# Optimization experiments

Hardware: AMD Instinct MI355X
Metric: run time of the kernel (lower is better)

Reference implementation:

```python
import jax, jax.numpy as jnp
import numpy as np

EMBED_DIM = 1024
NUM_HEADS = 16
D_K = EMBED_DIM // NUM_HEADS


def setup_inputs() -> dict:
    key = jax.random.key(0)
    ks = jax.random.split(key, 9)
    s = 1.0 / np.sqrt(EMBED_DIM)
    x = jax.random.normal(ks[0], (4, 2048, EMBED_DIM), dtype=jnp.float32)
    # nn.Linear weights stored as [out, in]; we keep [in, out] for x @ W
    W_q = jax.random.uniform(ks[1], (EMBED_DIM, EMBED_DIM), jnp.float32, -s, s)
    b_q = jax.random.uniform(ks[2], (EMBED_DIM,), jnp.float32, -s, s)
    W_k = jax.random.uniform(ks[3], (EMBED_DIM, EMBED_DIM), jnp.float32, -s, s)
    b_k = jax.random.uniform(ks[4], (EMBED_DIM,), jnp.float32, -s, s)
    W_v = jax.random.uniform(ks[5], (EMBED_DIM, EMBED_DIM), jnp.float32, -s, s)
    b_v = jax.random.uniform(ks[6], (EMBED_DIM,), jnp.float32, -s, s)
    W_o = jax.random.uniform(ks[7], (EMBED_DIM, EMBED_DIM), jnp.float32, -s, s)
    b_o = jax.random.uniform(ks[8], (EMBED_DIM,), jnp.float32, -s, s)
    return {"x": x, "W_q": W_q, "b_q": b_q, "W_k": W_k, "b_k": b_k,
            "W_v": W_v, "b_v": b_v, "W_o": W_o, "b_o": b_o}


def reference(x, W_q, b_q, W_k, b_k, W_v, b_v, W_o, b_o):
    B, N, _ = x.shape
    # QKV projections, split into heads: [B, H, N, d_k]
    def proj(W, b):
        return (x @ W + b).reshape(B, N, NUM_HEADS, D_K).transpose(0, 2, 1, 3)
    Q, K, V = proj(W_q, b_q), proj(W_k, b_k), proj(W_v, b_v)
    scale = 1.0 / np.sqrt(D_K).astype(np.float32)
    scores = jnp.einsum('bhqd,bhkd->bhqk', Q, K) * scale  # [B,H,N,N]
    weights = jax.nn.softmax(scores, axis=-1)
    # dropout is identity in eval mode
    attn = jnp.einsum('bhqk,bhkd->bhqd', weights, V)  # [B,H,N,d_k]
    attn = attn.transpose(0, 2, 1, 3).reshape(B, N, EMBED_DIM)
    return attn @ W_o + b_o
```

## Files before the change

kernel.cpp:

```cpp
#include <hip/hip_runtime.h>

typedef __bf16 bf16;
typedef __attribute__((ext_vector_type(8))) __bf16 bf16x8;
typedef __attribute__((ext_vector_type(4))) __bf16 bf16x4;
typedef __attribute__((ext_vector_type(4))) float f32x4;

static __device__ __forceinline__ f32x4 mfma16(bf16x8 a, bf16x8 b, f32x4 c) {
    return __builtin_amdgcn_mfma_f32_16x16x32_bf16(a, b, c, 0, 0, 0);
}

static __device__ __forceinline__ void gll16(const bf16* g, bf16* l) {
    __builtin_amdgcn_global_load_lds(
        (const __attribute__((address_space(1))) unsigned int*)g,
        (__attribute__((address_space(3))) unsigned int*)l, 16, 0, 0);
}

__global__ __launch_bounds__(256) void xcvt_kernel(
    const float* __restrict__ x, bf16* __restrict__ xb)
{
    size_t i = ((size_t)blockIdx.x * 256 + threadIdx.x) * 8;
    float4 a0 = *(const float4*)&x[i];
    float4 a1 = *(const float4*)&x[i + 4];
    bf16x8 v = {(bf16)a0.x, (bf16)a0.y, (bf16)a0.z, (bf16)a0.w,
                (bf16)a1.x, (bf16)a1.y, (bf16)a1.z, (bf16)a1.w};
    *(bf16x8*)&xb[i] = v;
}

__global__ __launch_bounds__(256) void wtrans_kernel(
    const float* __restrict__ Wq, const float* __restrict__ Wk,
    const float* __restrict__ Wv, const float* __restrict__ Wo,
    bf16* __restrict__ WTqkv, bf16* __restrict__ WTo)
{
    __shared__ bf16 tile[64][65];
    const int bid = blockIdx.x;
    const int mi = bid >> 8;
    const int t  = bid & 255;
    const int tr = t >> 4;
    const int tc = t & 15;
    const int tid = threadIdx.x;

    const float* src = (mi == 0) ? Wq : (mi == 1) ? Wk : (mi == 2) ? Wv : Wo;
    bf16* dst = (mi < 3) ? (WTqkv + (size_t)mi * 1024 * 1024) : WTo;

    #pragma unroll
    for (int i = 0; i < 16; i++) {
        int idx = i * 256 + tid;
        int rl = idx >> 6, cl = idx & 63;
        tile[rl][cl] = (bf16)src[(size_t)(tr * 64 + rl) * 1024 + tc * 64 + cl];
    }
    __syncthreads();
    #pragma unroll
    for (int i = 0; i < 16; i++) {
        int idx = i * 256 + tid;
        int rl = idx >> 6, cl = idx & 63;
        dst[(size_t)(tc * 64 + rl) * 1024 + tr * 64 + cl] = tile[cl][rl];
    }
}

__global__ void biascat_kernel(const float* __restrict__ bq, const float* __restrict__ bk,
                               const float* __restrict__ bv, float* __restrict__ dst)
{
    int i = blockIdx.x * 256 + threadIdx.x;
    if (i < 1024) dst[i] = bq[i];
    else if (i < 2048) dst[i] = bk[i - 1024];
    else dst[i] = bv[i - 2048];
}

#define QSCALE 0.18033688011112043f
__global__ __launch_bounds__(256) void gemm_bf16_kernel(
    const bf16* __restrict__ A, const bf16* __restrict__ BT,
    const float* __restrict__ bias, bf16* __restrict__ C,
    int M, int N, int K, int scaleQ)
{
    __shared__ bf16 sA[128 * 32];
    __shared__ bf16 sB[128 * 32];
    const int tid  = threadIdx.x;
    const int lane = tid & 63;
    const int wave = tid >> 6;
    const int quad = lane >> 4;
    const int l15  = lane & 15;
    const int wm = (wave >> 1) * 64;
    const int wn = (wave & 1) * 64;
    const int m0 = blockIdx.y * 128;
    const int n0 = blockIdx.x * 128;

    const f32x4 fzero = {0.f, 0.f, 0.f, 0.f};
    f32x4 acc[4][4];
    #pragma unroll
    for (int i = 0; i < 4; i++)
        #pragma unroll
        for (int j = 0; j < 4; j++) acc[i][j] = fzero;

    float bv[4];
    #pragma unroll
    for (int nc = 0; nc < 4; nc++) bv[nc] = bias[n0 + wn + nc * 16 + l15];

    const int rA = lane >> 2;
    const int cA = (lane & 3) * 8;

    for (int k0 = 0; k0 < K; k0 += 32) {
        #pragma unroll
        for (int p = 0; p < 2; p++) {
            int r16 = (wave * 2 + p) * 16;
            gll16(&A[(size_t)(m0 + r16 + rA) * K + k0 + cA], &sA[r16 * 32]);
            gll16(&BT[(size_t)(n0 + r16 + rA) * K + k0 + cA], &sB[r16 * 32]);
        }
        __syncthreads();

        bf16x8 aF[4], bF[4];
        #pragma unroll
        for (int mc = 0; mc < 4; mc++)
            aF[mc] = *(const bf16x8*)&sA[(wm + mc * 16 + l15) * 32 + quad * 8];
        #pragma unroll
        for (int nc = 0; nc < 4; nc++)
            bF[nc] = *(const bf16x8*)&sB[(wn + nc * 16 + l15) * 32 + quad * 8];

        #pragma unroll
        for (int mc = 0; mc < 4; mc++)
            #pragma unroll
            for (int nc = 0; nc < 4; nc++)
                acc[mc][nc] = mfma16(aF[mc], bF[nc], acc[mc][nc]);
        __syncthreads();
    }

    const float sc = (scaleQ && n0 < 1024) ? QSCALE : 1.0f;
    #pragma unroll
    for (int mc = 0; mc < 4; mc++) {
        #pragma unroll
        for (int reg = 0; reg < 4; reg++) {
            int row = m0 + wm + mc * 16 + quad * 4 + reg;
            size_t base = (size_t)row * N + n0 + wn;
            #pragma unroll
            for (int nc = 0; nc < 4; nc++)
                C[base + nc * 16 + l15] = (bf16)((acc[mc][nc][reg] + bv[nc]) * sc);
        }
    }
}

__global__ __launch_bounds__(256) void gemm_bf16_f32out_kernel(
    const bf16* __restrict__ A, const bf16* __restrict__ BT,
    const float* __restrict__ bias, float* __restrict__ C,
    int M, int N, int K)
{
    __shared__ bf16 sA[128 * 32];
    __shared__ bf16 sB[128 * 32];
    const int tid  = threadIdx.x;
    const int lane = tid & 63;
    const int wave = tid >> 6;
    const int quad = lane >> 4;
    const int l15  = lane & 15;
    const int wm = (wave >> 1) * 64;
    const int wn = (wave & 1) * 64;
    const int m0 = blockIdx.y * 128;
    const int n0 = blockIdx.x * 128;

    const f32x4 fzero = {0.f, 0.f, 0.f, 0.f};
    f32x4 acc[4][4];
    #pragma unroll
    for (int i = 0; i < 4; i++)
        #pragma unroll
        for (int j = 0; j < 4; j++) acc[i][j] = fzero;

    float bv[4];
    #pragma unroll
    for (int nc = 0; nc < 4; nc++) bv[nc] = bias[n0 + wn + nc * 16 + l15];

    const int rA = lane >> 2;
    const int cA = (lane & 3) * 8;

    for (int k0 = 0; k0 < K; k0 += 32) {
        #pragma unroll
        for (int p = 0; p < 2; p++) {
            int r16 = (wave * 2 + p) * 16;
            gll16(&A[(size_t)(m0 + r16 + rA) * K + k0 + cA], &sA[r16 * 32]);
            gll16(&BT[(size_t)(n0 + r16 + rA) * K + k0 + cA], &sB[r16 * 32]);
        }
        __syncthreads();

        bf16x8 aF[4], bF[4];
        #pragma unroll
        for (int mc = 0; mc < 4; mc++)
            aF[mc] = *(const bf16x8*)&sA[(wm + mc * 16 + l15) * 32 + quad * 8];
        #pragma unroll
        for (int nc = 0; nc < 4; nc++)
            bF[nc] = *(const bf16x8*)&sB[(wn + nc * 16 + l15) * 32 + quad * 8];

        #pragma unroll
        for (int mc = 0; mc < 4; mc++)
            #pragma unroll
            for (int nc = 0; nc < 4; nc++)
                acc[mc][nc] = mfma16(aF[mc], bF[nc], acc[mc][nc]);
        __syncthreads();
    }

    #pragma unroll
    for (int mc = 0; mc < 4; mc++) {
        #pragma unroll
        for (int reg = 0; reg < 4; reg++) {
            int row = m0 + wm + mc * 16 + quad * 4 + reg;
            size_t base = (size_t)row * N + n0 + wn;
            #pragma unroll
            for (int nc = 0; nc < 4; nc++)
                C[base + nc * 16 + l15] = acc[mc][nc][reg] + bv[nc];
        }
    }
}

__global__ __launch_bounds__(256) void vtrans_kernel(
    const bf16* __restrict__ QKVp, bf16* __restrict__ Vt)
{
    __shared__ bf16 tile[64][65];
    const int bid = blockIdx.x;
    const int bh = bid >> 5;
    const int nt = bid & 31;
    const int b = bh >> 4, h = bh & 15;
    const int tid = threadIdx.x;

    #pragma unroll
    for (int i = 0; i < 16; i++) {
        int idx = i * 256 + tid;
        int rl = idx >> 6, cl = idx & 63;
        tile[rl][cl] = QKVp[(size_t)(b * 2048 + nt * 64 + rl) * 3072 + 2048 + h * 64 + cl];
    }
    __syncthreads();
    #pragma unroll
    for (int i = 0; i < 16; i++) {
        int idx = i * 256 + tid;
        int rl = idx >> 6, cl = idx & 63;
        Vt[((size_t)bh * 64 + rl) * 2048 + nt * 64 + cl] = tile[cl][rl];
    }
}

__global__ __launch_bounds__(256) void attn_kernel(
    const bf16* __restrict__ QKV, const bf16* __restrict__ Vt,
    bf16* __restrict__ Opre)
{
    __shared__ bf16 sK[64 * 64];
    __shared__ bf16 sV[64 * 64];

    const int tid  = threadIdx.x;
    const int lane = tid & 63;
    const int w    = tid >> 6;
    const int quad = lane >> 4;
    const int l15  = lane & 15;
    const int bid = blockIdx.x;
    const int bh = bid >> 4;
    const int qt = bid & 15;
    const int b = bh >> 4, h = bh & 15;
    const int q0 = qt * 128;

    bf16x8 qF[2][2];
    #pragma unroll
    for (int g = 0; g < 2; g++) {
        size_t qrow = (size_t)(b * 2048 + q0 + w * 32 + g * 16 + l15) * 3072 + h * 64;
        qF[g][0] = *(const bf16x8*)&QKV[qrow + quad * 8];
        qF[g][1] = *(const bf16x8*)&QKV[qrow + 32 + quad * 8];
    }

    const f32x4 fzero = {0.f, 0.f, 0.f, 0.f};
    float psum[2] = {0.f, 0.f};
    f32x4 o[2][4];
    #pragma unroll
    for (int g = 0; g < 2; g++)
        #pragma unroll
        for (int mt = 0; mt < 4; mt++) o[g][mt] = fzero;

    const int srow = tid >> 3, sseg = tid & 7;
    const size_t kbase = (size_t)(b * 2048) * 3072 + 1024 + h * 64;
    const size_t vbase = (size_t)bh * 64 * 2048;

    const int swk = (l15 & 3) | (((l15 >> 2) & 1) << 2);
    const int swv = (l15 & 3) | (((l15 >> 3) & 1) << 2);

    for (int key0 = 0; key0 < 2048; key0 += 64) {
        #pragma unroll
        for (int p = 0; p < 2; p++) {
            int row = srow + p * 32;
            int sg = sseg ^ ((row & 3) | (((row >> 3) & 1) << 2));
            *(bf16x8*)&sK[row * 64 + sg * 8] =
                *(const bf16x8*)&QKV[kbase + (size_t)(key0 + row) * 3072 + sseg * 8];
            *(bf16x8*)&sV[row * 64 + sg * 8] =
                *(const bf16x8*)&Vt[vbase + (size_t)row * 2048 + key0 + sseg * 8];
        }
        __syncthreads();

        bf16x8 pB[2][2];
        #pragma unroll
        for (int c = 0; c < 4; c++) {
            int kr = ((l15 >> 2) << 3) + ((c & 1) << 2) + (l15 & 3) + ((c >> 1) << 5);
            bf16x8 kA0 = *(const bf16x8*)&sK[kr * 64 + ((quad ^ swk) * 8)];
            bf16x8 kA1 = *(const bf16x8*)&sK[kr * 64 + (((4 + quad) ^ swk) * 8)];
            #pragma unroll
            for (int g = 0; g < 2; g++) {
                f32x4 st = mfma16(kA0, qF[g][0], fzero);
                st = mfma16(kA1, qF[g][1], st);
                #pragma unroll
                for (int r = 0; r < 4; r++) {
                    float p = __builtin_amdgcn_exp2f(st[r]);
                    psum[g] += p;
                    pB[g][c >> 1][(c & 1) * 4 + r] = (bf16)p;
                }
            }
        }

        #pragma unroll
        for (int mt = 0; mt < 4; mt++) {
            int vr = mt * 16 + l15;
            bf16x8 vA0 = *(const bf16x8*)&sV[vr * 64 + ((quad ^ swv) * 8)];
            bf16x8 vA1 = *(const bf16x8*)&sV[vr * 64 + (((4 + quad) ^ swv) * 8)];
            #pragma unroll
            for (int g = 0; g < 2; g++) {
                o[g][mt] = mfma16(vA0, pB[g][0], o[g][mt]);
                o[g][mt] = mfma16(vA1, pB[g][1], o[g][mt]);
            }
        }
        __syncthreads();
    }

    #pragma unroll
    for (int g = 0; g < 2; g++) {
        float t = psum[g];
        t += __shfl_xor(t, 16);
        t += __shfl_xor(t, 32);
        float inv = 1.0f / t;
        size_t obase = (size_t)(b * 2048 + q0 + w * 32 + g * 16 + l15) * 1024 + h * 64;
        #pragma unroll
        for (int mt = 0; mt < 4; mt++) {
            bf16x4 ov = {(bf16)(o[g][mt][0] * inv), (bf16)(o[g][mt][1] * inv),
                         (bf16)(o[g][mt][2] * inv), (bf16)(o[g][mt][3] * inv)};
            *(bf16x4*)&Opre[obase + mt * 16 + quad * 4] = ov;
        }
    }
}

extern "C" void kernel_launch(void* const* d_in, const int* in_sizes, int n_in,
                              void* d_out, int out_size, void* d_ws, size_t ws_size,
                              hipStream_t stream)
{
    const float* x  = (const float*)d_in[0];
    const float* Wq = (const float*)d_in[1];
    const float* bq = (const float*)d_in[2];
    const float* Wk = (const float*)d_in[3];
    const float* bk = (const float*)d_in[4];
    const float* Wv = (const float*)d_in[5];
    const float* bv = (const float*)d_in[6];
    const float* Wo = (const float*)d_in[7];
    const float* bo = (const float*)d_in[8];
    float* out = (float*)d_out;

    bf16* WTqkv = (bf16*)d_ws;
    bf16* WTo   = WTqkv + (size_t)3072 * 1024;
    float* bcat = (float*)(WTo + (size_t)1024 * 1024);
    bf16* QKVp  = (bf16*)(bcat + 4096);
    bf16* Vt    = QKVp + (size_t)8192 * 3072;
    bf16* Apre  = Vt + (size_t)64 * 64 * 2048;
    bf16* xb    = Apre;
    (void)ws_size; (void)n_in; (void)in_sizes; (void)out_size;

    xcvt_kernel<<<4096, 256, 0, stream>>>(x, xb);
    wtrans_kernel<<<1024, 256, 0, stream>>>(Wq, Wk, Wv, Wo, WTqkv, WTo);
    biascat_kernel<<<12, 256, 0, stream>>>(bq, bk, bv, bcat);
    gemm_bf16_kernel<<<dim3(24, 64), 256, 0, stream>>>(xb, WTqkv, bcat, QKVp, 8192, 3072, 1024, 1);
    vtrans_kernel<<<2048, 256, 0, stream>>>(QKVp, Vt);
    attn_kernel<<<1024, 256, 0, stream>>>(QKVp, Vt, Apre);
    gemm_bf16_f32out_kernel<<<dim3(8, 64), 256, 0, stream>>>(Apre, WTo, bo, out, 8192, 1024, 1024);
}
```

Measured before the change: 310.4 us.

## Double-buffer K/V tiles in attention with register prefetch and MFMA priority

The attention kernel now double-buffers its K and V shared-memory tiles. The next tile is loaded from global memory into registers before computing on the current tile, then written to the other LDS buffer afterwards, which removes one barrier per iteration and hides global load latency. It also raises wave priority around the MFMA sequences with s_setprio. The cost is twice the LDS and extra registers for staging, which may lower occupancy.

```diff
diff --git a/kernel.cpp b/kernel.cpp
--- a/kernel.cpp
+++ b/kernel.cpp
@@ -235,8 +235,8 @@
     const bf16* __restrict__ QKV, const bf16* __restrict__ Vt,
     bf16* __restrict__ Opre)
 {
-    __shared__ bf16 sK[64 * 64];
-    __shared__ bf16 sV[64 * 64];
+    __shared__ bf16 sK[2][64 * 64];
+    __shared__ bf16 sV[2][64 * 64];
 
     const int tid  = threadIdx.x;
     const int lane = tid & 63;
@@ -268,32 +268,40 @@
     const int srow = tid >> 3, sseg = tid & 7;
     const size_t kbase = (size_t)(b * 2048) * 3072 + 1024 + h * 64;
     const size_t vbase = (size_t)bh * 64 * 2048;
+    const int sgsw = sseg ^ ((srow & 3) | (((srow >> 3) & 1) << 2));
 
     const int swk = (l15 & 3) | (((l15 >> 2) & 1) << 2);
     const int swv = (l15 & 3) | (((l15 >> 3) & 1) << 2);
 
-    for (int key0 = 0; key0 < 2048; key0 += 64) {
-        #pragma unroll
-        for (int p = 0; p < 2; p++) {
-            int row = srow + p * 32;
-            int sg = sseg ^ ((row & 3) | (((row >> 3) & 1) << 2));
-            *(bf16x8*)&sK[row * 64 + sg * 8] =
-                *(const bf16x8*)&QKV[kbase + (size_t)(key0 + row) * 3072 + sseg * 8];
-            *(bf16x8*)&sV[row * 64 + sg * 8] =
-                *(const bf16x8*)&Vt[vbase + (size_t)row * 2048 + key0 + sseg * 8];
-        }
-        __syncthreads();
-
+    bf16x8 stK[2], stV[2];
+
+    #pragma unroll
+    for (int p = 0; p < 2; p++) {
+        int row = srow + p * 32;
+        stK[p] = *(const bf16x8*)&QKV[kbase + (size_t)row * 3072 + sseg * 8];
+        stV[p] = *(const bf16x8*)&Vt[vbase + (size_t)row * 2048 + sseg * 8];
+    }
+    #pragma unroll
+    for (int p = 0; p < 2; p++) {
+        int row = srow + p * 32;
+        *(bf16x8*)&sK[0][row * 64 + sgsw * 8] = stK[p];
+        *(bf16x8*)&sV[0][row * 64 + sgsw * 8] = stV[p];
+    }
+    __syncthreads();
+
+    auto compute_tile = [&](const bf16* sKc, const bf16* sVc) {
         bf16x8 pB[2][2];
         #pragma unroll
         for (int c = 0; c < 4; c++) {
             int kr = ((l15 >> 2) << 3) + ((c & 1) << 2) + (l15 & 3) + ((c >> 1) << 5);
-            bf16x8 kA0 = *(const bf16x8*)&sK[kr * 64 + ((quad ^ swk) * 8)];
-            bf16x8 kA1 = *(const bf16x8*)&sK[kr * 64 + (((4 + quad) ^ swk) * 8)];
+            bf16x8 kA0 = *(const bf16x8*)&sKc[kr * 64 + ((quad ^ swk) * 8)];
+            bf16x8 kA1 = *(const bf16x8*)&sKc[kr * 64 + (((4 + quad) ^ swk) * 8)];
             #pragma unroll
             for (int g = 0; g < 2; g++) {
+                __builtin_amdgcn_s_setprio(1);
                 f32x4 st = mfma16(kA0, qF[g][0], fzero);
                 st = mfma16(kA1, qF[g][1], st);
+                __builtin_amdgcn_s_setprio(0);
                 #pragma unroll
                 for (int r = 0; r < 4; r++) {
                     float p = __builtin_amdgcn_exp2f(st[r]);
@@ -302,20 +310,44 @@
                 }
             }
         }
-
         #pragma unroll
         for (int mt = 0; mt < 4; mt++) {
             int vr = mt * 16 + l15;
-            bf16x8 vA0 = *(const bf16x8*)&sV[vr * 64 + ((quad ^ swv) * 8)];
-            bf16x8 vA1 = *(const bf16x8*)&sV[vr * 64 + (((4 + quad) ^ swv) * 8)];
+            bf16x8 vA0 = *(const bf16x8*)&sVc[vr * 64 + ((quad ^ swv) * 8)];
+            bf16x8 vA1 = *(const bf16x8*)&sVc[vr * 64 + (((4 + quad) ^ swv) * 8)];
+            __builtin_amdgcn_s_setprio(1);
             #pragma unroll
             for (int g = 0; g < 2; g++) {
                 o[g][mt] = mfma16(vA0, pB[g][0], o[g][mt]);
                 o[g][mt] = mfma16(vA1, pB[g][1], o[g][mt]);
             }
-        }
-        __syncthreads();
-    }
+            __builtin_amdgcn_s_setprio(0);
+        }
+    };
+
+    int cur = 0;
+    for (int t = 0; t < 31; t++) {
+        const int key0 = (t + 1) * 64;
+        #pragma unroll
+        for (int p = 0; p < 2; p++) {
+            int row = srow + p * 32;
+            stK[p] = *(const bf16x8*)&QKV[kbase + (size_t)(key0 + row) * 3072 + sseg * 8];
+            stV[p] = *(const bf16x8*)&Vt[vbase + (size_t)row * 2048 + key0 + sseg * 8];
+        }
+        __builtin_amdgcn_sched_barrier(0);
+
+        compute_tile(sK[cur], sV[cur]);
+
+        #pragma unroll
+        for (int p = 0; p < 2; p++) {
+            int row = srow + p * 32;
+            *(bf16x8*)&sK[cur ^ 1][row * 64 + sgsw * 8] = stK[p];
+            *(bf16x8*)&sV[cur ^ 1][row * 64 + sgsw * 8] = stV[p];
+        }
+        __syncthreads();
+        cur ^= 1;
+    }
+    compute_tile(sK[cur], sV[cur]);
 
     #pragma unroll
     for (int g = 0; g < 2; g++) {
```

Measured after the change: 299.3 us. -3.6%, faster.
